# Performance work log

Hardware: AMD Instinct MI355X
Metric: run time of the kernel (lower is better)

Reference implementation:

```python
import jax, jax.numpy as jnp
import numpy as np
from jax import lax


def setup_inputs() -> dict:
    key = jax.random.key(0)
    k1, k2 = jax.random.split(key)
    B, C, H, W = 64, 2, 256, 256
    logits = jax.random.normal(k1, (B, C, H, W), dtype=jnp.float32)
    mask = jnp.ones((B, H, W), dtype=jnp.float32)  # unused by the original math, kept for fidelity
    transitions = jax.random.normal(k2, (C, C), dtype=jnp.float32)
    return {"logits": logits, "mask": mask, "transitions": transitions}


def reference(logits, mask, transitions):
    B, C, H, W = logits.shape
    T = H * W
    # [B, C, H, W] -> [B, T, C] emission scores (matches permute(0,2,3,1).view)
    emits = jnp.transpose(logits, (0, 2, 3, 1)).reshape(B, T, C)

    # CRF forward algorithm: alpha_t[j] = logsumexp_i(alpha_{t-1}[i] + trans[j, i]) + emit[t, j]
    alpha0 = emits[:, 0, :]  # [B, C]
    emits_t = jnp.transpose(emits, (1, 0, 2))  # [T, B, C] for scan

    def step(alpha, emit_t):
        # alpha: [B, C] (over i), transitions[j, i] broadcast -> [B, j, i]
        new_alpha = jax.nn.logsumexp(alpha[:, None, :] + transitions[None, :, :], axis=-1) + emit_t
        return new_alpha, None

    alpha, _ = lax.scan(step, alpha0, emits_t[1:])
    log_likelihood = jax.nn.logsumexp(alpha, axis=1).sum()
    loss = -log_likelihood / B

    # decode: argmax over classes; torch views result as (B*H*W, 1)
    decoded = jnp.argmax(emits.reshape(-1, C), axis=1).reshape(-1, 1)
    return loss, decoded
```

## Files before the change

kernel.cpp:

```cpp
#include <hip/hip_runtime.h>
#include <math.h>


#define T_LEN   65536
#define SEG     4096
#define CH_L    16
#define NT      256
#define NSEG    16
#define NBATCH  64

__device__ __forceinline__ float lse2(float a, float b) {
    float m = fmaxf(a, b);
    float d = fminf(a, b) - m;
    return m + __builtin_amdgcn_logf(1.0f + __builtin_amdgcn_exp2f(d));
}

__global__ __launch_bounds__(NT) void crf_scan_kernel(
    const float* __restrict__ logits,
    const float* __restrict__ trans,
    float* __restrict__ out,
    float4* __restrict__ wsM)
{
    __shared__ float s0[SEG + SEG / 16];
    __shared__ float s1[SEG + SEG / 16];
    __shared__ float4 red[NT];

    const int blk = blockIdx.x;
    const int b   = blk >> 4;
    const int seg = blk & (NSEG - 1);
    const int tid = threadIdx.x;
    const float K = 1.4426950408889634f;

    const float* l0 = logits + (size_t)b * (2 * T_LEN) + (size_t)seg * SEG;
    const float* l1 = l0 + T_LEN;
    float* dec = out + 1 + (size_t)b * T_LEN + (size_t)seg * SEG;

    #pragma unroll
    for (int it = 0; it < SEG / (NT * 4); ++it) {
        const int idx = it * NT * 4 + tid * 4;
        const float4 a = *(const float4*)(l0 + idx);
        const float4 c = *(const float4*)(l1 + idx);
        dec[idx + 0] = (a.x >= c.x) ? 0.0f : 1.0f;
        dec[idx + 1] = (a.y >= c.y) ? 0.0f : 1.0f;
        dec[idx + 2] = (a.z >= c.z) ? 0.0f : 1.0f;
        dec[idx + 3] = (a.w >= c.w) ? 0.0f : 1.0f;
        const int li = idx + (idx >> 4);
        s0[li + 0] = a.x * K; s0[li + 1] = a.y * K; s0[li + 2] = a.z * K; s0[li + 3] = a.w * K;
        s1[li + 0] = c.x * K; s1[li + 1] = c.y * K; s1[li + 2] = c.z * K; s1[li + 3] = c.w * K;
    }

    const float t00 = trans[0] * K, t01 = trans[1] * K;
    const float t10 = trans[2] * K, t11 = trans[3] * K;
    __syncthreads();

    const int lb = tid * 17;
    float e0 = s0[lb], e1 = s1[lb];
    float m00, m01, m10, m11;
    if (seg == 0 && tid == 0) {
        m00 = e0; m11 = e1; m01 = -1e30f; m10 = -1e30f;
    } else {
        m00 = t00 + e0; m01 = t01 + e0;
        m10 = t10 + e1; m11 = t11 + e1;
    }
    #pragma unroll
    for (int j = 1; j < CH_L; ++j) {
        e0 = s0[lb + j]; e1 = s1[lb + j];
        float n00 = e0 + lse2(t00 + m00, t01 + m10);
        float n01 = e0 + lse2(t00 + m01, t01 + m11);
        float n10 = e1 + lse2(t10 + m00, t11 + m10);
        float n11 = e1 + lse2(t10 + m01, t11 + m11);
        m00 = n00; m01 = n01; m10 = n10; m11 = n11;
    }

    red[tid] = make_float4(m00, m01, m10, m11);
    __syncthreads();
    for (int s = NT / 2; s >= 1; s >>= 1) {
        if (tid < s) {
            float4 A  = red[tid + s];
            float4 Bm = red[tid];
            float c00 = lse2(A.x + Bm.x, A.y + Bm.z);
            float c01 = lse2(A.x + Bm.y, A.y + Bm.w);
            float c10 = lse2(A.z + Bm.x, A.w + Bm.z);
            float c11 = lse2(A.z + Bm.y, A.w + Bm.w);
            red[tid] = make_float4(c00, c01, c10, c11);
        }
        __syncthreads();
    }
    if (tid == 0) wsM[blk] = red[0];
}

__global__ __launch_bounds__(64) void crf_final_kernel(
    const float4* __restrict__ wsM, float* __restrict__ out)
{
    const int b = threadIdx.x;
    float4 Acc = wsM[b * NSEG];
    #pragma unroll
    for (int s = 1; s < NSEG; ++s) {
        float4 A = wsM[b * NSEG + s];
        float c00 = lse2(A.x + Acc.x, A.y + Acc.z);
        float c01 = lse2(A.x + Acc.y, A.y + Acc.w);
        float c10 = lse2(A.z + Acc.x, A.w + Acc.z);
        float c11 = lse2(A.z + Acc.y, A.w + Acc.w);
        Acc = make_float4(c00, c01, c10, c11);
    }
    float ll2 = lse2(lse2(Acc.x, Acc.y), lse2(Acc.z, Acc.w));
    #pragma unroll
    for (int off = 32; off >= 1; off >>= 1) ll2 += __shfl_xor(ll2, off);
    if (b == 0) out[0] = -(0.6931471805599453f * ll2) * (1.0f / (float)NBATCH);
}

extern "C" void kernel_launch(void* const* d_in, const int* in_sizes, int n_in,
                              void* d_out, int out_size, void* d_ws, size_t ws_size,
                              hipStream_t stream) {
    const float* logits = (const float*)d_in[0];
    const float* trans  = (const float*)d_in[2];
    float* out  = (float*)d_out;
    float4* wsM = (float4*)d_ws;

    crf_scan_kernel<<<NBATCH * NSEG, NT, 0, stream>>>(logits, trans, out, wsM);
    crf_final_kernel<<<1, 64, 0, stream>>>(wsM, out);
}
```

Baseline: 96.55 us.

## Use wave shuffles for segment reduction, interleave emissions in LDS, vectorize decode stores

```diff
diff --git a/kernel.cpp b/kernel.cpp
--- a/kernel.cpp
+++ b/kernel.cpp
@@ -15,15 +15,16 @@
     return m + __builtin_amdgcn_logf(1.0f + __builtin_amdgcn_exp2f(d));
 }
 
+struct __attribute__((packed, aligned(4))) F4 { float x, y, z, w; };
+
 __global__ __launch_bounds__(NT) void crf_scan_kernel(
     const float* __restrict__ logits,
     const float* __restrict__ trans,
     float* __restrict__ out,
     float4* __restrict__ wsM)
 {
-    __shared__ float s0[SEG + SEG / 16];
-    __shared__ float s1[SEG + SEG / 16];
-    __shared__ float4 red[NT];
+    __shared__ float2 sE[SEG + SEG / 16];
+    __shared__ float4 red4[NT / 64];
 
     const int blk = blockIdx.x;
     const int b   = blk >> 4;
@@ -40,13 +41,17 @@
         const int idx = it * NT * 4 + tid * 4;
         const float4 a = *(const float4*)(l0 + idx);
         const float4 c = *(const float4*)(l1 + idx);
-        dec[idx + 0] = (a.x >= c.x) ? 0.0f : 1.0f;
-        dec[idx + 1] = (a.y >= c.y) ? 0.0f : 1.0f;
-        dec[idx + 2] = (a.z >= c.z) ? 0.0f : 1.0f;
-        dec[idx + 3] = (a.w >= c.w) ? 0.0f : 1.0f;
+        F4 dv;
+        dv.x = (a.x >= c.x) ? 0.0f : 1.0f;
+        dv.y = (a.y >= c.y) ? 0.0f : 1.0f;
+        dv.z = (a.z >= c.z) ? 0.0f : 1.0f;
+        dv.w = (a.w >= c.w) ? 0.0f : 1.0f;
+        __builtin_memcpy(dec + idx, &dv, sizeof(F4));
         const int li = idx + (idx >> 4);
-        s0[li + 0] = a.x * K; s0[li + 1] = a.y * K; s0[li + 2] = a.z * K; s0[li + 3] = a.w * K;
-        s1[li + 0] = c.x * K; s1[li + 1] = c.y * K; s1[li + 2] = c.z * K; s1[li + 3] = c.w * K;
+        sE[li + 0] = make_float2(a.x * K, c.x * K);
+        sE[li + 1] = make_float2(a.y * K, c.y * K);
+        sE[li + 2] = make_float2(a.z * K, c.z * K);
+        sE[li + 3] = make_float2(a.w * K, c.w * K);
     }
 
     const float t00 = trans[0] * K, t01 = trans[1] * K;
@@ -54,56 +59,83 @@
     __syncthreads();
 
     const int lb = tid * 17;
-    float e0 = s0[lb], e1 = s1[lb];
+    float2 e = sE[lb];
     float m00, m01, m10, m11;
     if (seg == 0 && tid == 0) {
-        m00 = e0; m11 = e1; m01 = -1e30f; m10 = -1e30f;
+        m00 = e.x; m11 = e.y; m01 = -1e30f; m10 = -1e30f;
     } else {
-        m00 = t00 + e0; m01 = t01 + e0;
-        m10 = t10 + e1; m11 = t11 + e1;
+        m00 = t00 + e.x; m01 = t01 + e.x;
+        m10 = t10 + e.y; m11 = t11 + e.y;
     }
     #pragma unroll
     for (int j = 1; j < CH_L; ++j) {
-        e0 = s0[lb + j]; e1 = s1[lb + j];
-        float n00 = e0 + lse2(t00 + m00, t01 + m10);
-        float n01 = e0 + lse2(t00 + m01, t01 + m11);
-        float n10 = e1 + lse2(t10 + m00, t11 + m10);
-        float n11 = e1 + lse2(t10 + m01, t11 + m11);
+        e = sE[lb + j];
+        float n00 = e.x + lse2(t00 + m00, t01 + m10);
+        float n01 = e.x + lse2(t00 + m01, t01 + m11);
+        float n10 = e.y + lse2(t10 + m00, t11 + m10);
+        float n11 = e.y + lse2(t10 + m01, t11 + m11);
         m00 = n00; m01 = n01; m10 = n10; m11 = n11;
     }
 
-    red[tid] = make_float4(m00, m01, m10, m11);
+    const int lane = tid & 63;
+    #pragma unroll
+    for (int s = 1; s < 64; s <<= 1) {
+        float px = __shfl_xor(m00, s);
+        float py = __shfl_xor(m01, s);
+        float pz = __shfl_xor(m10, s);
+        float pw = __shfl_xor(m11, s);
+        const bool up = (lane & s) != 0;
+        float lx = up ? m00 : px, ly = up ? m01 : py;
+        float lz = up ? m10 : pz, lw = up ? m11 : pw;
+        float ex = up ? px : m00, ey = up ? py : m01;
+        float ez = up ? pz : m10, ew = up ? pw : m11;
+        m00 = lse2(lx + ex, ly + ez);
+        m01 = lse2(lx + ey, ly + ew);
+        m10 = lse2(lz + ex, lw + ez);
+        m11 = lse2(lz + ey, lw + ew);
+    }
+    if (lane == 0) red4[tid >> 6] = make_float4(m00, m01, m10, m11);
     __syncthreads();
-    for (int s = NT / 2; s >= 1; s >>= 1) {
-        if (tid < s) {
-            float4 A  = red[tid + s];
-            float4 Bm = red[tid];
-            float c00 = lse2(A.x + Bm.x, A.y + Bm.z);
-            float c01 = lse2(A.x + Bm.y, A.y + Bm.w);
-            float c10 = lse2(A.z + Bm.x, A.w + Bm.z);
-            float c11 = lse2(A.z + Bm.y, A.w + Bm.w);
-            red[tid] = make_float4(c00, c01, c10, c11);
-        }
-        __syncthreads();
+    if (tid == 0) {
+        float4 A = red4[0], Bv = red4[1], Cv = red4[2], Dv = red4[3];
+        float4 P01, P23, M;
+        P01.x = lse2(Bv.x + A.x, Bv.y + A.z);
+        P01.y = lse2(Bv.x + A.y, Bv.y + A.w);
+        P01.z = lse2(Bv.z + A.x, Bv.w + A.z);
+        P01.w = lse2(Bv.z + A.y, Bv.w + A.w);
+        P23.x = lse2(Dv.x + Cv.x, Dv.y + Cv.z);
+        P23.y = lse2(Dv.x + Cv.y, Dv.y + Cv.w);
+        P23.z = lse2(Dv.z + Cv.x, Dv.w + Cv.z);
+        P23.w = lse2(Dv.z + Cv.y, Dv.w + Cv.w);
+        M.x = lse2(P23.x + P01.x, P23.y + P01.z);
+        M.y = lse2(P23.x + P01.y, P23.y + P01.w);
+        M.z = lse2(P23.z + P01.x, P23.w + P01.z);
+        M.w = lse2(P23.z + P01.y, P23.w + P01.w);
+        wsM[seg * NBATCH + b] = M;
     }
-    if (tid == 0) wsM[blk] = red[0];
 }
 
 __global__ __launch_bounds__(64) void crf_final_kernel(
     const float4* __restrict__ wsM, float* __restrict__ out)
 {
     const int b = threadIdx.x;
-    float4 Acc = wsM[b * NSEG];
+    float4 M[NSEG];
     #pragma unroll
-    for (int s = 1; s < NSEG; ++s) {
-        float4 A = wsM[b * NSEG + s];
-        float c00 = lse2(A.x + Acc.x, A.y + Acc.z);
-        float c01 = lse2(A.x + Acc.y, A.y + Acc.w);
-        float c10 = lse2(A.z + Acc.x, A.w + Acc.z);
-        float c11 = lse2(A.z + Acc.y, A.w + Acc.w);
-        Acc = make_float4(c00, c01, c10, c11);
+    for (int s = 0; s < NSEG; ++s) M[s] = wsM[s * NBATCH + b];
+    #pragma unroll
+    for (int n = NSEG / 2; n >= 1; n >>= 1) {
+        #pragma unroll
+        for (int i = 0; i < n; ++i) {
+            float4 E = M[2 * i], L = M[2 * i + 1];
+            float4 R;
+            R.x = lse2(L.x + E.x, L.y + E.z);
+            R.y = lse2(L.x + E.y, L.y + E.w);
+            R.z = lse2(L.z + E.x, L.w + E.z);
+            R.w = lse2(L.z + E.y, L.w + E.w);
+            M[i] = R;
+        }
     }
-    float ll2 = lse2(lse2(Acc.x, Acc.y), lse2(Acc.z, Acc.w));
+    float ll2 = lse2(lse2(M[0].x, M[0].y), lse2(M[0].z, M[0].w));
     #pragma unroll
     for (int off = 32; off >= 1; off >>= 1) ll2 += __shfl_xor(ll2, off);
     if (b == 0) out[0] = -(0.6931471805599453f * ll2) * (1.0f / (float)NBATCH);
```

New measurement: 96.39 us. No clear change (-0.2%).
